# Kernel optimization log

Hardware: AMD Instinct MI355X
Metric: run time of the kernel (lower is better)

Reference implementation:

```python
import jax, jax.numpy as jnp
import numpy as np

KH = KW = 3
PAD = 1

def _patches(x):
    # x: [B, C, H, W] -> periodic pad then 3x3 patches [B, C, KH, KW, H, W]
    B, C, H, W = x.shape
    xp = jnp.pad(x, ((0, 0), (0, 0), (PAD, PAD), (PAD, PAD)), mode='wrap')
    rows = []
    for i in range(KH):
        cols = [xp[:, :, i:i + H, j:j + W] for j in range(KW)]
        rows.append(jnp.stack(cols, axis=2))  # [B, C, KW, H, W]
    return jnp.stack(rows, axis=2)  # [B, C, KH, KW, H, W]

def setup_inputs() -> dict:
    key = jax.random.key(0)
    k1, k2, k3 = jax.random.split(key, 3)
    B, C, O, H, W = 16, 64, 64, 128, 128
    input = jax.random.normal(k1, (B, C, H, W), dtype=jnp.float32)
    weight = jax.random.normal(k2, (B, C * KH * KW, O), dtype=jnp.float32) * 0.05
    bias = jax.random.normal(k3, (B, O), dtype=jnp.float32) * 0.05
    return {"input": input, "weight": weight, "bias": bias}

def reference(input, weight, bias):
    B, C, H, W = input.shape
    O = weight.shape[-1]
    p = _patches(input)  # [B, C, KH, KW, H, W]
    w = weight.reshape(B, C, KH, KW, O)
    # per-sample dynamic conv: contract over (C, KH, KW)
    y = jnp.einsum('bcijhw,bcijo->bohw', p, w)
    return y + bias[:, :, None, None]
```

## Files before the change

### kernel.cpp

```cpp
#include <hip/hip_runtime.h>
#include <stdint.h>

#define B_N 16
#define C_N 64
#define O_N 64
#define H_N 128
#define W_N 128

typedef short bf16x8 __attribute__((ext_vector_type(8)));
typedef float f32x4 __attribute__((ext_vector_type(4)));
typedef unsigned short u16;
typedef u16 u16x4 __attribute__((ext_vector_type(4)));

__device__ __forceinline__ u16 f2bf(float f) {
    uint32_t u = __float_as_uint(f);
    u += 0x7FFFu + ((u >> 16) & 1u);
    return (u16)(u >> 16);
}

__device__ __forceinline__ int swz(int w) { return (w & 7) << 4; }

__global__ __launch_bounds__(256) void prep_weights(const float* __restrict__ wt,
                                                    u16* __restrict__ wf) {
    int idx = blockIdx.x * 256 + threadIdx.x;
    int e = idx;
    int o4 = e & 15; e >>= 4;
    int ij = e % 9;  e /= 9;
    int c  = e & 63; e >>= 6;
    int b  = e;
    f32x4 v = *reinterpret_cast<const f32x4*>(
        wt + ((size_t)b * 576 + (size_t)c * 9 + ij) * 64 + o4 * 4);
    const int cs = c >> 5, lgc = (c >> 3) & 3, j8 = c & 7;
#pragma unroll
    for (int k = 0; k < 4; ++k) {
        int o = o4 * 4 + k;
        int of = o >> 4, lrc = o & 15;
        size_t dst = ((size_t)((((b * 9 + ij) * 2 + cs) * 4 + of) * 64 + lgc * 16 + lrc)) * 8 + j8;
        wf[dst] = f2bf(v[k]);
    }
}

__global__ __launch_bounds__(512, 2) void conv_main(const float* __restrict__ x,
                                                    const u16* __restrict__ wf,
                                                    const float* __restrict__ bias,
                                                    float* __restrict__ y) {
    extern __shared__ u16 smem[];
    u16* xl = smem;
    u16* wl = smem + 32768;

    const int lid = (blockIdx.x & 7) * 32 + (blockIdx.x >> 3);
    const int b   = lid >> 4;
    const int h0  = (lid & 15) * 8;
    const int tid = threadIdx.x;
    const int wid = tid >> 6;
    const int l   = tid & 63;
    const int wave_m = wid >> 1;
    const int wave_n = wid & 1;
    const int m0 = wave_m * 32;
    const int o0 = wave_n * 32;
    const int lr = l & 15;
    const int lg = l >> 4;

    const int w4 = tid & 31;
    const int cq = tid >> 5;
    const float* xb = x + (size_t)b * (64 * 128 * 128);
    const u16* wfb  = wf + (size_t)b * 36864;

#pragma unroll
    for (int k = 0; k < 9; ++k) {
        bf16x8 v = *reinterpret_cast<const bf16x8*>(wfb + k * 4096 + tid * 8);
        *reinterpret_cast<bf16x8*>(wl + k * 4096 + tid * 8) = v;
    }

    const float bv0 = bias[b * 64 + o0 + lr];
    const float bv1 = bias[b * 64 + o0 + 16 + lr];

    auto ldrow = [&](int s, f32x4* d) {
        int hr = (h0 + s + 127) & 127;
        const float* src = xb + ((size_t)cq * 4 * 128 + hr) * 128 + w4 * 4;
        d[0] = *reinterpret_cast<const f32x4*>(src);
        d[1] = *reinterpret_cast<const f32x4*>(src + 16384);
        d[2] = *reinterpret_cast<const f32x4*>(src + 32768);
        d[3] = *reinterpret_cast<const f32x4*>(src + 49152);
    };
    auto wrrow = [&](int s, const f32x4* d) {
#pragma unroll
        for (int j = 0; j < 4; ++j) {
            int w = w4 * 4 + j;
            u16x4 pk;
            pk.x = f2bf(d[0][j]); pk.y = f2bf(d[1][j]);
            pk.z = f2bf(d[2][j]); pk.w = f2bf(d[3][j]);
            int byte = (s & 3) * 16384 + w * 128 + cq * 8;
            byte ^= swz(w);
            *reinterpret_cast<u16x4*>(reinterpret_cast<char*>(xl) + byte) = pk;
        }
    };

    f32x4 st[4];
#pragma unroll
    for (int s = 0; s < 3; ++s) { ldrow(s, st); wrrow(s, st); }
    __syncthreads();

#pragma unroll 1
    for (int r = 0; r < 8; ++r) {
        f32x4 acc[2][2];
#pragma unroll
        for (int mf = 0; mf < 2; ++mf)
#pragma unroll
            for (int nf = 0; nf < 2; ++nf)
                acc[mf][nf] = (f32x4){0.f, 0.f, 0.f, 0.f};

#pragma unroll
        for (int ij = 0; ij < 9; ++ij) {
            if (ij == 2 && r < 7) ldrow(r + 3, st);
            if (ij == 6 && r < 7) wrrow(r + 3, st);

            const int i = ij / 3;
            const int jsh = ij % 3 - 1;
            const int rbase = ((r + i) & 3) * 16384;
#pragma unroll
            for (int cs = 0; cs < 2; ++cs) {
                const int cb = cs * 64 + lg * 16;
                bf16x8 afr[2], bfr[2];
#pragma unroll
                for (int nf = 0; nf < 2; ++nf)
                    bfr[nf] = *reinterpret_cast<const bf16x8*>(
                        wl + (size_t)(((ij * 2 + cs) * 4 + wave_n * 2 + nf) * 64 + l) * 8);
#pragma unroll
                for (int mf = 0; mf < 2; ++mf) {
                    int w = (m0 + mf * 16 + lr + jsh + 128) & 127;
                    int byte = rbase + w * 128 + cb;
                    byte ^= swz(w);
                    afr[mf] = *reinterpret_cast<const bf16x8*>(
                        reinterpret_cast<const char*>(xl) + byte);
                }
#pragma unroll
                for (int mf = 0; mf < 2; ++mf) {
                    acc[mf][0] = __builtin_amdgcn_mfma_f32_16x16x32_bf16(afr[mf], bfr[0], acc[mf][0], 0, 0, 0);
                    acc[mf][1] = __builtin_amdgcn_mfma_f32_16x16x32_bf16(afr[mf], bfr[1], acc[mf][1], 0, 0, 0);
                }
            }
        }

        const int h = h0 + r;
#pragma unroll
        for (int nf = 0; nf < 2; ++nf) {
            int o = o0 + nf * 16 + lr;
            float bv = nf ? bv1 : bv0;
#pragma unroll
            for (int mf = 0; mf < 2; ++mf) {
                int w0 = m0 + mf * 16 + lg * 4;
                float* dst = y + (((size_t)b * 64 + o) * 128 + h) * 128 + w0;
                f32x4 out;
                out[0] = acc[mf][nf][0] + bv;
                out[1] = acc[mf][nf][1] + bv;
                out[2] = acc[mf][nf][2] + bv;
                out[3] = acc[mf][nf][3] + bv;
                *reinterpret_cast<f32x4*>(dst) = out;
            }
        }
        if (r < 7) __syncthreads();
    }
}

__global__ void naive_conv(const float* __restrict__ x, const float* __restrict__ wt,
                           const float* __restrict__ bias, float* __restrict__ y) {
    int w = threadIdx.x;
    int h = blockIdx.x & 127;
    int o = (blockIdx.x >> 7) & 63;
    int b = blockIdx.x >> 13;
    float s = bias[b * 64 + o];
    for (int c = 0; c < 64; ++c)
        for (int i = 0; i < 3; ++i)
            for (int j = 0; j < 3; ++j) {
                int hh = (h + i + 127) & 127;
                int ww = (w + j + 127) & 127;
                s += x[(((size_t)b * 64 + c) * 128 + hh) * 128 + ww] *
                     wt[((size_t)b * 576 + (size_t)(c * 9 + i * 3 + j)) * 64 + o];
            }
    y[(((size_t)b * 64 + o) * 128 + h) * 128 + w] = s;
}

extern "C" void kernel_launch(void* const* d_in, const int* in_sizes, int n_in,
                              void* d_out, int out_size, void* d_ws, size_t ws_size,
                              hipStream_t stream) {
    const float* x    = (const float*)d_in[0];
    const float* wt   = (const float*)d_in[1];
    const float* bias = (const float*)d_in[2];
    float* y = (float*)d_out;

    const size_t WF_ELEMS = (size_t)B_N * 9 * 2 * 4 * 64 * 8;
    const size_t WF_BYTES = WF_ELEMS * sizeof(u16);
    const int DYN_LDS = 4 * 128 * 64 * 2 + 9 * 2 * 4 * 64 * 8 * 2;

    static int attr_done = 0;
    if (!attr_done) {
        (void)hipFuncSetAttribute(reinterpret_cast<const void*>(conv_main),
                                  hipFuncAttributeMaxDynamicSharedMemorySize, DYN_LDS);
        attr_done = 1;
    }

    if (ws_size >= WF_BYTES) {
        u16* wf = (u16*)d_ws;
        hipLaunchKernelGGL(prep_weights, dim3(576), dim3(256), 0, stream, wt, wf);
        hipLaunchKernelGGL(conv_main, dim3(B_N * H_N / 8), dim3(512), DYN_LDS, stream, x, wf, bias, y);
    } else {
        hipLaunchKernelGGL(naive_conv, dim3(B_N * O_N * H_N), dim3(128), 0, stream, x, wt, bias, y);
    }
}
```

Baseline: 39.07 us.

## Keep per-wave weight fragments in registers instead of LDS

Each wave now loads its bf16 weight fragments for all 9 taps and both channel halves straight from global memory into a register array. The shared-memory copy of the weights and the per-iteration LDS reads of the B operand are gone. The three halo input rows are fetched into separate registers before the weight loads so the two overlap, and LDS shrinks to a static 64KB buffer. The cost is heavy register pressure (about 144 VGPRs just for weights), which under the 512-thread, 2-blocks launch bound may cause spills or lower occupancy.

```diff
diff --git a/kernel.cpp b/kernel.cpp
--- a/kernel.cpp
+++ b/kernel.cpp
@@ -44,9 +44,7 @@
                                                     const u16* __restrict__ wf,
                                                     const float* __restrict__ bias,
                                                     float* __restrict__ y) {
-    extern __shared__ u16 smem[];
-    u16* xl = smem;
-    u16* wl = smem + 32768;
+    __shared__ u16 xl[4 * 128 * 64];
 
     const int lid = (blockIdx.x & 7) * 32 + (blockIdx.x >> 3);
     const int b   = lid >> 4;
@@ -66,15 +64,6 @@
     const float* xb = x + (size_t)b * (64 * 128 * 128);
     const u16* wfb  = wf + (size_t)b * 36864;
 
-#pragma unroll
-    for (int k = 0; k < 9; ++k) {
-        bf16x8 v = *reinterpret_cast<const bf16x8*>(wfb + k * 4096 + tid * 8);
-        *reinterpret_cast<bf16x8*>(wl + k * 4096 + tid * 8) = v;
-    }
-
-    const float bv0 = bias[b * 64 + o0 + lr];
-    const float bv1 = bias[b * 64 + o0 + 16 + lr];
-
     auto ldrow = [&](int s, f32x4* d) {
         int hr = (h0 + s + 127) & 127;
         const float* src = xb + ((size_t)cq * 4 * 128 + hr) * 128 + w4 * 4;
@@ -96,11 +85,26 @@
         }
     };
 
+    f32x4 s0[4], s1[4], s2[4];
+    ldrow(0, s0); ldrow(1, s1); ldrow(2, s2);
+
+    bf16x8 wreg[9][2][2];
+#pragma unroll
+    for (int ij = 0; ij < 9; ++ij)
+#pragma unroll
+        for (int cs = 0; cs < 2; ++cs)
+#pragma unroll
+            for (int nf = 0; nf < 2; ++nf)
+                wreg[ij][cs][nf] = *reinterpret_cast<const bf16x8*>(
+                    wfb + (size_t)(((ij * 2 + cs) * 4 + wave_n * 2 + nf) * 64 + l) * 8);
+
+    const float bv0 = bias[b * 64 + o0 + lr];
+    const float bv1 = bias[b * 64 + o0 + 16 + lr];
+
+    wrrow(0, s0); wrrow(1, s1); wrrow(2, s2);
+    __syncthreads();
+
     f32x4 st[4];
-#pragma unroll
-    for (int s = 0; s < 3; ++s) { ldrow(s, st); wrrow(s, st); }
-    __syncthreads();
-
 #pragma unroll 1
     for (int r = 0; r < 8; ++r) {
         f32x4 acc[2][2];
@@ -121,11 +125,7 @@
 #pragma unroll
             for (int cs = 0; cs < 2; ++cs) {
                 const int cb = cs * 64 + lg * 16;
-                bf16x8 afr[2], bfr[2];
-#pragma unroll
-                for (int nf = 0; nf < 2; ++nf)
-                    bfr[nf] = *reinterpret_cast<const bf16x8*>(
-                        wl + (size_t)(((ij * 2 + cs) * 4 + wave_n * 2 + nf) * 64 + l) * 8);
+                bf16x8 afr[2];
 #pragma unroll
                 for (int mf = 0; mf < 2; ++mf) {
                     int w = (m0 + mf * 16 + lr + jsh + 128) & 127;
@@ -136,8 +136,8 @@
                 }
 #pragma unroll
                 for (int mf = 0; mf < 2; ++mf) {
-                    acc[mf][0] = __builtin_amdgcn_mfma_f32_16x16x32_bf16(afr[mf], bfr[0], acc[mf][0], 0, 0, 0);
-                    acc[mf][1] = __builtin_amdgcn_mfma_f32_16x16x32_bf16(afr[mf], bfr[1], acc[mf][1], 0, 0, 0);
+                    acc[mf][0] = __builtin_amdgcn_mfma_f32_16x16x32_bf16(afr[mf], wreg[ij][cs][0], acc[mf][0], 0, 0, 0);
+                    acc[mf][1] = __builtin_amdgcn_mfma_f32_16x16x32_bf16(afr[mf], wreg[ij][cs][1], acc[mf][1], 0, 0, 0);
                 }
             }
         }
@@ -191,19 +191,11 @@
 
     const size_t WF_ELEMS = (size_t)B_N * 9 * 2 * 4 * 64 * 8;
     const size_t WF_BYTES = WF_ELEMS * sizeof(u16);
-    const int DYN_LDS = 4 * 128 * 64 * 2 + 9 * 2 * 4 * 64 * 8 * 2;
-
-    static int attr_done = 0;
-    if (!attr_done) {
-        (void)hipFuncSetAttribute(reinterpret_cast<const void*>(conv_main),
-                                  hipFuncAttributeMaxDynamicSharedMemorySize, DYN_LDS);
-        attr_done = 1;
-    }
 
     if (ws_size >= WF_BYTES) {
         u16* wf = (u16*)d_ws;
         hipLaunchKernelGGL(prep_weights, dim3(576), dim3(256), 0, stream, wt, wf);
-        hipLaunchKernelGGL(conv_main, dim3(B_N * H_N / 8), dim3(512), DYN_LDS, stream, x, wf, bias, y);
+        hipLaunchKernelGGL(conv_main, dim3(B_N * H_N / 8), dim3(512), 0, stream, x, wf, bias, y);
     } else {
         hipLaunchKernelGGL(naive_conv, dim3(B_N * O_N * H_N), dim3(128), 0, stream, x, wt, bias, y);
     }
```

After: 38.79 us. Within noise of the previous version (-0.7%).
